# Kernel optimization log

Hardware: AMD Instinct MI355X
Metric: run time of the kernel (lower is better)

## Reference

```python
import jax, jax.numpy as jnp
import numpy as np

HIDDEN = 4096
NUM_HEADS = 32
HEAD_DIM = HIDDEN // NUM_HEADS  # 128
ROPE_THETA = 10000.0
B, S = 1, 2048


def setup_inputs() -> dict:
    key = jax.random.key(0)
    k1, k2, k3, k4, k5 = jax.random.split(key, 5)
    positions = jnp.broadcast_to(jnp.arange(S, dtype=jnp.int64), (B, S))
    hidden_states = jax.random.normal(k1, (B, S, HIDDEN), dtype=jnp.float32)
    scale = 1.0 / np.sqrt(HIDDEN)
    Wqkv = jax.random.normal(k2, (HIDDEN, 3 * HIDDEN), dtype=jnp.float32) * scale
    bqkv = jax.random.normal(k3, (3 * HIDDEN,), dtype=jnp.float32) * 0.01
    Wo = jax.random.normal(k4, (HIDDEN, HIDDEN), dtype=jnp.float32) * scale
    bo = jax.random.normal(k5, (HIDDEN,), dtype=jnp.float32) * 0.01
    return {"positions": positions, "hidden_states": hidden_states,
            "Wqkv": Wqkv, "bqkv": bqkv, "Wo": Wo, "bo": bo}


def _apply_rope(x, positions):
    # x: [B, S, H, D]; neox-style (rotate halves) rotary embedding
    half = HEAD_DIM // 2
    inv_freq = 1.0 / (ROPE_THETA ** (jnp.arange(0, HEAD_DIM, 2, dtype=jnp.float32) / HEAD_DIM))
    freqs = positions.astype(jnp.float32)[..., None] * inv_freq  # [B, S, half]
    cos = jnp.cos(freqs)[:, :, None, :]  # [B, S, 1, half]
    sin = jnp.sin(freqs)[:, :, None, :]
    x1, x2 = x[..., :half], x[..., half:]
    return jnp.concatenate([x1 * cos - x2 * sin, x2 * cos + x1 * sin], axis=-1)


def reference(positions, hidden_states, Wqkv, bqkv, Wo, bo):
    qkv = hidden_states @ Wqkv + bqkv  # [B, S, 3*HIDDEN]
    q, k, v = jnp.split(qkv, 3, axis=-1)
    q = q.reshape(B, S, NUM_HEADS, HEAD_DIM)
    k = k.reshape(B, S, NUM_HEADS, HEAD_DIM)
    v = v.reshape(B, S, NUM_HEADS, HEAD_DIM)
    q = _apply_rope(q, positions)
    k = _apply_rope(k, positions)
    scaling = HEAD_DIM ** -0.5
    scores = jnp.einsum('bshd,bthd->bhst', q, k) * scaling  # [B, H, S, S]
    causal = jnp.tril(jnp.ones((S, S), dtype=bool))
    scores = jnp.where(causal, scores, jnp.finfo(scores.dtype).min)
    attn = jax.nn.softmax(scores, axis=-1)
    out = jnp.einsum('bhst,bthd->bshd', attn, v).reshape(B, S, HIDDEN)
    return out @ Wo + bo
```

## Files before the change

kernel.cpp:

```cpp
#include <hip/hip_runtime.h>

using short8  = __attribute__((ext_vector_type(8))) short;
using floatx4 = __attribute__((ext_vector_type(4))) float;

__device__ inline float b2f(ushort u) {
  union { unsigned u; float f; } x; x.u = ((unsigned)u) << 16; return x.f;
}
__device__ inline ushort f2b(float f) {
  union { float f; unsigned u; } x; x.f = f;
  unsigned r = x.u + 0x7fffu + ((x.u >> 16) & 1u);
  return (ushort)(r >> 16);
}

__device__ __forceinline__ void gl_lds16(const void* g, void* l) {
  __builtin_amdgcn_global_load_lds(
      (const __attribute__((address_space(1))) unsigned*)(unsigned long long)g,
      (__attribute__((address_space(3))) unsigned*)(unsigned)(unsigned long long)l,
      16, 0, 0);
}

__global__ __launch_bounds__(256) void cvt_f32_bf16(
    const float* __restrict__ in, ushort* __restrict__ out, int n4) {
  const int i = blockIdx.x * 256 + threadIdx.x;
  if (i < n4) {
    const float4 v = ((const float4*)in)[i];
    ushort4 o;
    o.x = f2b(v.x); o.y = f2b(v.y); o.z = f2b(v.z); o.w = f2b(v.w);
    ((ushort4*)out)[i] = o;
  }
}

__global__ __launch_bounds__(256) void transpose_f32_bf16(
    const float* __restrict__ W, int ldw, ushort* __restrict__ Wt, int K) {
  __shared__ ushort tile[64 * 72];
  const int kb = blockIdx.y * 64, nb = blockIdx.x * 64;
  const int t = threadIdx.x;
  {
    const int tn = t & 63, tk4 = t >> 6;
#pragma unroll
    for (int i = 0; i < 16; ++i) {
      const int k = tk4 + i * 4;
      tile[k * 72 + tn] = f2b(W[(size_t)(kb + k) * ldw + (nb + tn)]);
    }
  }
  __syncthreads();
  {
    const int tk = t & 63, tn4 = t >> 6;
#pragma unroll
    for (int i = 0; i < 16; ++i) {
      const int n = tn4 + i * 4;
      Wt[(size_t)(nb + n) * K + (kb + tk)] = tile[tk * 72 + n];
    }
  }
}

__global__ __launch_bounds__(256) void transpose_v_bf16(
    const ushort* __restrict__ qkv, ushort* __restrict__ vT) {
  __shared__ ushort tile[64 * 68];
  const int s0 = blockIdx.y * 64, c0 = blockIdx.x * 64;
  const int t = threadIdx.x;
  {
    const int tc = t & 63, ts4 = t >> 6;
#pragma unroll
    for (int i = 0; i < 16; ++i) {
      const int s = ts4 + i * 4;
      tile[s * 68 + tc] = qkv[(size_t)(s0 + s) * 12288 + 8192 + c0 + tc];
    }
  }
  __syncthreads();
  {
    const int ts = t & 63, tc4 = t >> 6;
#pragma unroll
    for (int i = 0; i < 16; ++i) {
      const int c = tc4 + i * 4;
      vT[(size_t)(c0 + c) * 2048 + (s0 + ts)] = tile[ts * 68 + c];
    }
  }
}

template <bool F32OUT>
__global__ __launch_bounds__(256) void gemm_bt_bias(
    const ushort* __restrict__ A, const ushort* __restrict__ Bt,
    const float* __restrict__ bias, void* __restrict__ Cout,
    int ldc, int M, int N, int K) {
  __shared__ ushort sA[128 * 64];
  __shared__ ushort sB[128 * 64];
  const int tid = threadIdx.x;
  const int lane = tid & 63, w = tid >> 6;
  const int lm = lane & 15, lq = lane >> 4;
  const int wr = w >> 1, wc = w & 1;
  const int m0 = blockIdx.y * 128, n0 = blockIdx.x * 128;
  floatx4 acc[4][4] = {};

  const int srow = w * 32 + (lane >> 3);
  const int scol = (lane & 7) * 8;
  const ushort* Ag = A + (size_t)(m0 + srow) * K + scol;
  const ushort* Bg = Bt + (size_t)(n0 + srow) * K + scol;

  for (int k0 = 0; k0 < K; k0 += 64) {
    __syncthreads();
#pragma unroll
    for (int j = 0; j < 4; ++j) {
      gl_lds16(Ag + (size_t)j * 8 * K + k0, &sA[(w * 32 + j * 8) * 64]);
      gl_lds16(Bg + (size_t)j * 8 * K + k0, &sB[(w * 32 + j * 8) * 64]);
    }
    __syncthreads();
#pragma unroll
    for (int ks = 0; ks < 2; ++ks) {
      short8 af[4], bf[4];
#pragma unroll
      for (int i = 0; i < 4; ++i)
        af[i] = *(const short8*)&sA[(wr * 64 + i * 16 + lm) * 64 + ks * 32 + lq * 8];
#pragma unroll
      for (int j = 0; j < 4; ++j)
        bf[j] = *(const short8*)&sB[(wc * 64 + j * 16 + lm) * 64 + ks * 32 + lq * 8];
#pragma unroll
      for (int i = 0; i < 4; ++i)
#pragma unroll
        for (int j = 0; j < 4; ++j)
          acc[i][j] = __builtin_amdgcn_mfma_f32_16x16x32_bf16(af[i], bf[j], acc[i][j], 0, 0, 0);
    }
  }
#pragma unroll
  for (int i = 0; i < 4; ++i) {
#pragma unroll
    for (int j = 0; j < 4; ++j) {
      const int row = m0 + wr * 64 + i * 16 + lq * 4;
      const int col = n0 + wc * 64 + j * 16 + lm;
      const float bs = bias[col];
      if (F32OUT) {
        float* C = (float*)Cout;
#pragma unroll
        for (int r = 0; r < 4; ++r)
          C[(size_t)(row + r) * ldc + col] = acc[i][j][r] + bs;
      } else {
        ushort* C = (ushort*)Cout;
#pragma unroll
        for (int r = 0; r < 4; ++r)
          C[(size_t)(row + r) * ldc + col] = f2b(acc[i][j][r] + bs);
      }
    }
  }
}

__global__ __launch_bounds__(256) void rope_kernel(ushort* __restrict__ qkv) {
  const int s = blockIdx.x;
  const float pos = (float)s;
  for (int i = threadIdx.x; i < 2048; i += 256) {
    const int h = i >> 6, d = i & 63;
    const float inv_freq = exp2f(-(float)d * 0.20762050593045952f);
    const float f = pos * inv_freq;
    float sn, cs; sincosf(f, &sn, &cs);
    const size_t base = (size_t)s * 12288 + h * 128 + d;
    {
      float x1 = b2f(qkv[base]), x2 = b2f(qkv[base + 64]);
      qkv[base]      = f2b(x1 * cs - x2 * sn);
      qkv[base + 64] = f2b(x2 * cs + x1 * sn);
    }
    {
      const size_t kb = base + 4096;
      float x1 = b2f(qkv[kb]), x2 = b2f(qkv[kb + 64]);
      qkv[kb]      = f2b(x1 * cs - x2 * sn);
      qkv[kb + 64] = f2b(x2 * cs + x1 * sn);
    }
  }
}

__global__ __launch_bounds__(256) void flash_kernel(
    const ushort* __restrict__ qkv, const ushort* __restrict__ vT,
    ushort* __restrict__ attn) {
  constexpr int QKV = 12288;
  __shared__ ushort smem[20480];
  ushort* sK  = smem;
  ushort* sVt = smem + 8192;
  ushort* sP  = smem + 16384;

  const int h   = blockIdx.y;
  const int tid = threadIdx.x;
  const int lane = tid & 63, w = tid >> 6;
  const int lm = lane & 15, lq = lane >> 4;
  const int c16 = lane & 15, l4 = lane >> 4;
  const int c8  = lane & 7,  l3 = lane >> 3;
  const float sc = 0.08838834764831845f * 1.4426950408889634f;

  for (int qsel = 0; qsel < 2; ++qsel) {
    const int qt = qsel ? blockIdx.x : 31 - blockIdx.x;
    const int q0 = qt * 64;

    __syncthreads();
#pragma unroll
    for (int j = 0; j < 4; ++j) {
      const int row = w * 16 + j * 4 + l4;
      const int sw = c16 ^ (row & 7);
      gl_lds16(qkv + (size_t)(q0 + row) * QKV + h * 128 + sw * 8,
               &sK[(w * 16 + j * 4) * 128]);
    }
    __syncthreads();
    short8 aq[4];
#pragma unroll
    for (int kk = 0; kk < 4; ++kk)
      aq[kk] = *(const short8*)&sK[(w * 16 + lm) * 128 + (((kk * 4 + lq) ^ (lm & 7)) * 8)];

    floatx4 acco[8] = {};
    float mrun[4], lrun[4];
#pragma unroll
    for (int r = 0; r < 4; ++r) { mrun[r] = -1e30f; lrun[r] = 0.f; }

    const int nkv = qt + 1;
    for (int it = 0; it < nkv; ++it) {
      const int kv0 = it * 64;
      __syncthreads();
#pragma unroll
      for (int j = 0; j < 4; ++j) {
        const int row = w * 16 + j * 4 + l4;
        const int sw = c16 ^ (row & 7);
        gl_lds16(qkv + (size_t)(kv0 + row) * QKV + 4096 + h * 128 + sw * 8,
                 &sK[(w * 16 + j * 4) * 128]);
      }
#pragma unroll
      for (int j = 0; j < 4; ++j) {
        const int vrow = w * 32 + j * 8 + l3;
        const int sw = c8 ^ (vrow & 7);
        gl_lds16(vT + (size_t)(h * 128 + vrow) * 2048 + kv0 + sw * 8,
                 &sVt[(w * 32 + j * 8) * 64]);
      }
      __syncthreads();

      floatx4 accs[4] = {};
#pragma unroll
      for (int kk = 0; kk < 4; ++kk) {
        short8 bk[4];
#pragma unroll
        for (int nt = 0; nt < 4; ++nt)
          bk[nt] = *(const short8*)&sK[(nt * 16 + lm) * 128 + (((kk * 4 + lq) ^ (lm & 7)) * 8)];
#pragma unroll
        for (int nt = 0; nt < 4; ++nt)
          accs[nt] = __builtin_amdgcn_mfma_f32_16x16x32_bf16(aq[kk], bk[nt], accs[nt], 0, 0, 0);
      }

      const bool domask = (it == nkv - 1);
      float tmax[4];
#pragma unroll
      for (int r = 0; r < 4; ++r) tmax[r] = -1e30f;
#pragma unroll
      for (int nt = 0; nt < 4; ++nt)
#pragma unroll
        for (int r = 0; r < 4; ++r) {
          float v = accs[nt][r] * sc;
          if (domask) {
            const int qrow = q0 + w * 16 + lq * 4 + r;
            const int kcol = kv0 + nt * 16 + lm;
            if (kcol > qrow) v = -1e30f;
          }
          accs[nt][r] = v;
          tmax[r] = fmaxf(tmax[r], v);
        }
#pragma unroll
      for (int r = 0; r < 4; ++r) {
        float t = tmax[r];
#pragma unroll
        for (int off = 1; off < 16; off <<= 1) t = fmaxf(t, __shfl_xor(t, off, 64));
        const float mnew = fmaxf(mrun[r], t);
        const float alpha = exp2f(mrun[r] - mnew);
        mrun[r] = mnew;
        lrun[r] *= alpha;
#pragma unroll
        for (int nt = 0; nt < 8; ++nt) acco[nt][r] *= alpha;
      }
      float rsum[4] = {};
#pragma unroll
      for (int nt = 0; nt < 4; ++nt)
#pragma unroll
        for (int r = 0; r < 4; ++r) {
          const float p = exp2f(accs[nt][r] - mrun[r]);
          rsum[r] += p;
          sP[(w * 16 + lq * 4 + r) * 64 +
             (((2 * nt + (lm >> 3)) ^ ((lq * 4 + r) & 7)) * 8) + (lm & 7)] = f2b(p);
        }
#pragma unroll
      for (int r = 0; r < 4; ++r) {
        float t = rsum[r];
#pragma unroll
        for (int off = 1; off < 16; off <<= 1) t += __shfl_xor(t, off, 64);
        lrun[r] += t;
      }

#pragma unroll
      for (int ks = 0; ks < 2; ++ks) {
        const short8 ap = *(const short8*)&sP[(w * 16 + lm) * 64 + (((ks * 4 + lq) ^ (lm & 7)) * 8)];
#pragma unroll
        for (int nt = 0; nt < 8; ++nt) {
          const short8 bv = *(const short8*)&sVt[(nt * 16 + lm) * 64 + (((ks * 4 + lq) ^ (lm & 7)) * 8)];
          acco[nt] = __builtin_amdgcn_mfma_f32_16x16x32_bf16(ap, bv, acco[nt], 0, 0, 0);
        }
      }
    }

#pragma unroll
    for (int r = 0; r < 4; ++r) {
      const float inv = 1.0f / lrun[r];
      const int row = q0 + w * 16 + lq * 4 + r;
#pragma unroll
      for (int nt = 0; nt < 8; ++nt) {
        const int col = h * 128 + nt * 16 + lm;
        attn[(size_t)row * 4096 + col] = f2b(acco[nt][r] * inv);
      }
    }
  }
}

extern "C" void kernel_launch(void* const* d_in, const int* in_sizes, int n_in,
                              void* d_out, int out_size, void* d_ws, size_t ws_size,
                              hipStream_t stream) {
  const float* hidden = (const float*)d_in[1];
  const float* Wqkv   = (const float*)d_in[2];
  const float* bqkv   = (const float*)d_in[3];
  const float* Wo     = (const float*)d_in[4];
  const float* bo     = (const float*)d_in[5];

  ushort* ws   = (ushort*)d_ws;
  ushort* Wt   = ws;
  ushort* hb   = ws + (size_t)16777216;
  ushort* qkv  = ws + (size_t)25165824;
  ushort* attn = ws + (size_t)50331648;

  cvt_f32_bf16<<<8192, 256, 0, stream>>>(hidden, hb, 2097152);

  for (int c = 0; c < 3; ++c) {
    transpose_f32_bf16<<<dim3(64, 64), 256, 0, stream>>>(Wqkv + c * 4096, 12288, Wt, 4096);
    gemm_bt_bias<false><<<dim3(32, 16), 256, 0, stream>>>(
        hb, Wt, bqkv + c * 4096, (void*)(qkv + c * 4096), 12288, 2048, 4096, 4096);
  }

  rope_kernel<<<2048, 256, 0, stream>>>(qkv);
  transpose_v_bf16<<<dim3(64, 32), 256, 0, stream>>>(qkv, Wt);
  flash_kernel<<<dim3(16, 32), 256, 0, stream>>>(qkv, Wt, attn);

  transpose_f32_bf16<<<dim3(64, 64), 256, 0, stream>>>(Wo, 4096, Wt, 4096);
  gemm_bt_bias<true><<<dim3(32, 16), 256, 0, stream>>>(
      attn, Wt, bo, d_out, 4096, 2048, 4096, 4096);
}
```

Before: 870.1 us.

## Vectorize transposes and RoPE, give each flash block one query tile

The two transpose kernels switch to 16-byte vector global loads and stores, using an XOR-swizzled shared tile in place of padding. RoPE now handles 8 contiguous elements per thread with int4 loads and stores, with no strided loop. The flash kernel drops the pair of mirrored query tiles per block and launches twice as many blocks, one query tile each, ordered heaviest first. The last change raises parallelism but gives up the balanced per-block work of the pairing.

```diff
diff --git a/kernel.cpp b/kernel.cpp
--- a/kernel.cpp
+++ b/kernel.cpp
@@ -32,48 +32,69 @@
 
 __global__ __launch_bounds__(256) void transpose_f32_bf16(
     const float* __restrict__ W, int ldw, ushort* __restrict__ Wt, int K) {
-  __shared__ ushort tile[64 * 72];
+  __shared__ ushort tile[64 * 64];
   const int kb = blockIdx.y * 64, nb = blockIdx.x * 64;
   const int t = threadIdx.x;
   {
-    const int tn = t & 63, tk4 = t >> 6;
-#pragma unroll
-    for (int i = 0; i < 16; ++i) {
-      const int k = tk4 + i * 4;
-      tile[k * 72 + tn] = f2b(W[(size_t)(kb + k) * ldw + (nb + tn)]);
+    const int tn4 = t & 15;
+    const int tk  = t >> 4;
+#pragma unroll
+    for (int i = 0; i < 4; ++i) {
+      const int k = tk + i * 16;
+      const float4 v = *(const float4*)&W[(size_t)(kb + k) * ldw + nb + tn4 * 4];
+      ushort4 o; o.x = f2b(v.x); o.y = f2b(v.y); o.z = f2b(v.z); o.w = f2b(v.w);
+      const int c = tn4 ^ (k & 15);
+      *(ushort4*)&tile[k * 64 + c * 4] = o;
     }
   }
   __syncthreads();
   {
-    const int tk = t & 63, tn4 = t >> 6;
-#pragma unroll
-    for (int i = 0; i < 16; ++i) {
-      const int n = tn4 + i * 4;
-      Wt[(size_t)(nb + n) * K + (kb + tk)] = tile[tk * 72 + n];
+    const int kc = t & 7;
+    const int tn = t >> 3;
+#pragma unroll
+    for (int p = 0; p < 2; ++p) {
+      const int n = tn + p * 32;
+      union { int4 v; ushort u[8]; } o;
+#pragma unroll
+      for (int j = 0; j < 8; ++j) {
+        const int k = kc * 8 + j;
+        const int c = (n >> 2) ^ (k & 15);
+        o.u[j] = tile[k * 64 + c * 4 + (n & 3)];
+      }
+      *(int4*)&Wt[(size_t)(nb + n) * K + kb + kc * 8] = o.v;
     }
   }
 }
 
 __global__ __launch_bounds__(256) void transpose_v_bf16(
     const ushort* __restrict__ qkv, ushort* __restrict__ vT) {
-  __shared__ ushort tile[64 * 68];
+  __shared__ ushort tile[64 * 64];
   const int s0 = blockIdx.y * 64, c0 = blockIdx.x * 64;
   const int t = threadIdx.x;
   {
-    const int tc = t & 63, ts4 = t >> 6;
-#pragma unroll
-    for (int i = 0; i < 16; ++i) {
-      const int s = ts4 + i * 4;
-      tile[s * 68 + tc] = qkv[(size_t)(s0 + s) * 12288 + 8192 + c0 + tc];
+    const int tc8 = t & 7, ts = t >> 3;
+#pragma unroll
+    for (int p = 0; p < 2; ++p) {
+      const int s = ts + p * 32;
+      int4 x = *(const int4*)(qkv + (size_t)(s0 + s) * 12288 + 8192 + c0 + tc8 * 8);
+      const int c8 = tc8 ^ (s & 7) ^ ((s >> 3) & 7);
+      *(int4*)&tile[s * 64 + c8 * 8] = x;
     }
   }
   __syncthreads();
   {
-    const int ts = t & 63, tc4 = t >> 6;
-#pragma unroll
-    for (int i = 0; i < 16; ++i) {
-      const int c = tc4 + i * 4;
-      vT[(size_t)(c0 + c) * 2048 + (s0 + ts)] = tile[ts * 68 + c];
+    const int sc = t & 7, tc = t >> 3;
+#pragma unroll
+    for (int p = 0; p < 2; ++p) {
+      const int c = tc + p * 32;
+      union { int4 v; ushort u[8]; } o;
+#pragma unroll
+      for (int j = 0; j < 8; ++j) {
+        const int s = sc * 8 + j;
+        const int c8 = (c >> 3) ^ (s & 7) ^ ((s >> 3) & 7);
+        o.u[j] = tile[s * 64 + c8 * 8 + (c & 7)];
+      }
+      *(int4*)&vT[(size_t)(c0 + c) * 2048 + s0 + sc * 8] = o.v;
     }
   }
 }
@@ -146,24 +167,38 @@
 __global__ __launch_bounds__(256) void rope_kernel(ushort* __restrict__ qkv) {
   const int s = blockIdx.x;
   const float pos = (float)s;
-  for (int i = threadIdx.x; i < 2048; i += 256) {
-    const int h = i >> 6, d = i & 63;
-    const float inv_freq = exp2f(-(float)d * 0.20762050593045952f);
-    const float f = pos * inv_freq;
-    float sn, cs; sincosf(f, &sn, &cs);
-    const size_t base = (size_t)s * 12288 + h * 128 + d;
-    {
-      float x1 = b2f(qkv[base]), x2 = b2f(qkv[base + 64]);
-      qkv[base]      = f2b(x1 * cs - x2 * sn);
-      qkv[base + 64] = f2b(x2 * cs + x1 * sn);
-    }
-    {
-      const size_t kb = base + 4096;
-      float x1 = b2f(qkv[kb]), x2 = b2f(qkv[kb + 64]);
-      qkv[kb]      = f2b(x1 * cs - x2 * sn);
-      qkv[kb + 64] = f2b(x2 * cs + x1 * sn);
-    }
-  }
+  const int t = threadIdx.x;
+  const int h = t >> 3, d8 = (t & 7) * 8;
+  const size_t base = (size_t)s * 12288 + h * 128 + d8;
+  union U { int4 v; ushort u[8]; };
+  U q1, q2, k1, k2;
+  q1.v = *(const int4*)(qkv + base);
+  q2.v = *(const int4*)(qkv + base + 64);
+  k1.v = *(const int4*)(qkv + base + 4096);
+  k2.v = *(const int4*)(qkv + base + 4160);
+  float sn[8], cs[8];
+#pragma unroll
+  for (int j = 0; j < 8; ++j) {
+    const float inv_freq = exp2f(-(float)(d8 + j) * 0.20762050593045952f);
+    sincosf(pos * inv_freq, &sn[j], &cs[j]);
+  }
+  U o1, o2;
+#pragma unroll
+  for (int j = 0; j < 8; ++j) {
+    const float x1 = b2f(q1.u[j]), x2 = b2f(q2.u[j]);
+    o1.u[j] = f2b(x1 * cs[j] - x2 * sn[j]);
+    o2.u[j] = f2b(x2 * cs[j] + x1 * sn[j]);
+  }
+  *(int4*)(qkv + base)      = o1.v;
+  *(int4*)(qkv + base + 64) = o2.v;
+#pragma unroll
+  for (int j = 0; j < 8; ++j) {
+    const float x1 = b2f(k1.u[j]), x2 = b2f(k2.u[j]);
+    o1.u[j] = f2b(x1 * cs[j] - x2 * sn[j]);
+    o2.u[j] = f2b(x2 * cs[j] + x1 * sn[j]);
+  }
+  *(int4*)(qkv + base + 4096) = o1.v;
+  *(int4*)(qkv + base + 4160) = o2.v;
 }
 
 __global__ __launch_bounds__(256) void flash_kernel(
@@ -183,128 +218,125 @@
   const int c8  = lane & 7,  l3 = lane >> 3;
   const float sc = 0.08838834764831845f * 1.4426950408889634f;
 
-  for (int qsel = 0; qsel < 2; ++qsel) {
-    const int qt = qsel ? blockIdx.x : 31 - blockIdx.x;
-    const int q0 = qt * 64;
-
+  const int qt = 31 - blockIdx.x;
+  const int q0 = qt * 64;
+
+#pragma unroll
+  for (int j = 0; j < 4; ++j) {
+    const int row = w * 16 + j * 4 + l4;
+    const int sw = c16 ^ (row & 7);
+    gl_lds16(qkv + (size_t)(q0 + row) * QKV + h * 128 + sw * 8,
+             &sK[(w * 16 + j * 4) * 128]);
+  }
+  __syncthreads();
+  short8 aq[4];
+#pragma unroll
+  for (int kk = 0; kk < 4; ++kk)
+    aq[kk] = *(const short8*)&sK[(w * 16 + lm) * 128 + (((kk * 4 + lq) ^ (lm & 7)) * 8)];
+
+  floatx4 acco[8] = {};
+  float mrun[4], lrun[4];
+#pragma unroll
+  for (int r = 0; r < 4; ++r) { mrun[r] = -1e30f; lrun[r] = 0.f; }
+
+  const int nkv = qt + 1;
+  for (int it = 0; it < nkv; ++it) {
+    const int kv0 = it * 64;
     __syncthreads();
 #pragma unroll
     for (int j = 0; j < 4; ++j) {
       const int row = w * 16 + j * 4 + l4;
       const int sw = c16 ^ (row & 7);
-      gl_lds16(qkv + (size_t)(q0 + row) * QKV + h * 128 + sw * 8,
+      gl_lds16(qkv + (size_t)(kv0 + row) * QKV + 4096 + h * 128 + sw * 8,
                &sK[(w * 16 + j * 4) * 128]);
     }
+#pragma unroll
+    for (int j = 0; j < 4; ++j) {
+      const int vrow = w * 32 + j * 8 + l3;
+      const int sw = c8 ^ (vrow & 7);
+      gl_lds16(vT + (size_t)(h * 128 + vrow) * 2048 + kv0 + sw * 8,
+               &sVt[(w * 32 + j * 8) * 64]);
+    }
     __syncthreads();
-    short8 aq[4];
-#pragma unroll
-    for (int kk = 0; kk < 4; ++kk)
-      aq[kk] = *(const short8*)&sK[(w * 16 + lm) * 128 + (((kk * 4 + lq) ^ (lm & 7)) * 8)];
-
-    floatx4 acco[8] = {};
-    float mrun[4], lrun[4];
-#pragma unroll
-    for (int r = 0; r < 4; ++r) { mrun[r] = -1e30f; lrun[r] = 0.f; }
-
-    const int nkv = qt + 1;
-    for (int it = 0; it < nkv; ++it) {
-      const int kv0 = it * 64;
-      __syncthreads();
-#pragma unroll
-      for (int j = 0; j < 4; ++j) {
-        const int row = w * 16 + j * 4 + l4;
-        const int sw = c16 ^ (row & 7);
-        gl_lds16(qkv + (size_t)(kv0 + row) * QKV + 4096 + h * 128 + sw * 8,
-                 &sK[(w * 16 + j * 4) * 128]);
-      }
-#pragma unroll
-      for (int j = 0; j < 4; ++j) {
-        const int vrow = w * 32 + j * 8 + l3;
-        const int sw = c8 ^ (vrow & 7);
-        gl_lds16(vT + (size_t)(h * 128 + vrow) * 2048 + kv0 + sw * 8,
-                 &sVt[(w * 32 + j * 8) * 64]);
-      }
-      __syncthreads();
-
-      floatx4 accs[4] = {};
-#pragma unroll
-      for (int kk = 0; kk < 4; ++kk) {
-        short8 bk[4];
-#pragma unroll
-        for (int nt = 0; nt < 4; ++nt)
-          bk[nt] = *(const short8*)&sK[(nt * 16 + lm) * 128 + (((kk * 4 + lq) ^ (lm & 7)) * 8)];
-#pragma unroll
-        for (int nt = 0; nt < 4; ++nt)
-          accs[nt] = __builtin_amdgcn_mfma_f32_16x16x32_bf16(aq[kk], bk[nt], accs[nt], 0, 0, 0);
-      }
-
-      const bool domask = (it == nkv - 1);
-      float tmax[4];
-#pragma unroll
-      for (int r = 0; r < 4; ++r) tmax[r] = -1e30f;
+
+    floatx4 accs[4] = {};
+#pragma unroll
+    for (int kk = 0; kk < 4; ++kk) {
+      short8 bk[4];
 #pragma unroll
       for (int nt = 0; nt < 4; ++nt)
-#pragma unroll
-        for (int r = 0; r < 4; ++r) {
-          float v = accs[nt][r] * sc;
-          if (domask) {
-            const int qrow = q0 + w * 16 + lq * 4 + r;
-            const int kcol = kv0 + nt * 16 + lm;
-            if (kcol > qrow) v = -1e30f;
-          }
-          accs[nt][r] = v;
-          tmax[r] = fmaxf(tmax[r], v);
+        bk[nt] = *(const short8*)&sK[(nt * 16 + lm) * 128 + (((kk * 4 + lq) ^ (lm & 7)) * 8)];
+#pragma unroll
+      for (int nt = 0; nt < 4; ++nt)
+        accs[nt] = __builtin_amdgcn_mfma_f32_16x16x32_bf16(aq[kk], bk[nt], accs[nt], 0, 0, 0);
+    }
+
+    const bool domask = (it == nkv - 1);
+    float tmax[4];
+#pragma unroll
+    for (int r = 0; r < 4; ++r) tmax[r] = -1e30f;
+#pragma unroll
+    for (int nt = 0; nt < 4; ++nt)
+#pragma unroll
+      for (int r = 0; r < 4; ++r) {
+        float v = accs[nt][r] * sc;
+        if (domask) {
+          const int qrow = q0 + w * 16 + lq * 4 + r;
+          const int kcol = kv0 + nt * 16 + lm;
+          if (kcol > qrow) v = -1e30f;
         }
+        accs[nt][r] = v;
+        tmax[r] = fmaxf(tmax[r], v);
+      }
+#pragma unroll
+    for (int r = 0; r < 4; ++r) {
+      float t = tmax[r];
+#pragma unroll
+      for (int off = 1; off < 16; off <<= 1) t = fmaxf(t, __shfl_xor(t, off, 64));
+      const float mnew = fmaxf(mrun[r], t);
+      const float alpha = exp2f(mrun[r] - mnew);
+      mrun[r] = mnew;
+      lrun[r] *= alpha;
+#pragma unroll
+      for (int nt = 0; nt < 8; ++nt) acco[nt][r] *= alpha;
+    }
+    float rsum[4] = {};
+#pragma unroll
+    for (int nt = 0; nt < 4; ++nt)
 #pragma unroll
       for (int r = 0; r < 4; ++r) {
-        float t = tmax[r];
-#pragma unroll
-        for (int off = 1; off < 16; off <<= 1) t = fmaxf(t, __shfl_xor(t, off, 64));
-        const float mnew = fmaxf(mrun[r], t);
-        const float alpha = exp2f(mrun[r] - mnew);
-        mrun[r] = mnew;
-        lrun[r] *= alpha;
-#pragma unroll
-        for (int nt = 0; nt < 8; ++nt) acco[nt][r] *= alpha;
-      }
-      float rsum[4] = {};
-#pragma unroll
-      for (int nt = 0; nt < 4; ++nt)
-#pragma unroll
-        for (int r = 0; r < 4; ++r) {
-          const float p = exp2f(accs[nt][r] - mrun[r]);
-          rsum[r] += p;
-          sP[(w * 16 + lq * 4 + r) * 64 +
-             (((2 * nt + (lm >> 3)) ^ ((lq * 4 + r) & 7)) * 8) + (lm & 7)] = f2b(p);
-        }
-#pragma unroll
-      for (int r = 0; r < 4; ++r) {
-        float t = rsum[r];
-#pragma unroll
-        for (int off = 1; off < 16; off <<= 1) t += __shfl_xor(t, off, 64);
-        lrun[r] += t;
-      }
-
-#pragma unroll
-      for (int ks = 0; ks < 2; ++ks) {
-        const short8 ap = *(const short8*)&sP[(w * 16 + lm) * 64 + (((ks * 4 + lq) ^ (lm & 7)) * 8)];
-#pragma unroll
-        for (int nt = 0; nt < 8; ++nt) {
-          const short8 bv = *(const short8*)&sVt[(nt * 16 + lm) * 64 + (((ks * 4 + lq) ^ (lm & 7)) * 8)];
-          acco[nt] = __builtin_amdgcn_mfma_f32_16x16x32_bf16(ap, bv, acco[nt], 0, 0, 0);
-        }
-      }
-    }
-
+        const float p = exp2f(accs[nt][r] - mrun[r]);
+        rsum[r] += p;
+        sP[(w * 16 + lq * 4 + r) * 64 +
+           (((2 * nt + (lm >> 3)) ^ ((lq * 4 + r) & 7)) * 8) + (lm & 7)] = f2b(p);
+      }
 #pragma unroll
     for (int r = 0; r < 4; ++r) {
-      const float inv = 1.0f / lrun[r];
-      const int row = q0 + w * 16 + lq * 4 + r;
+      float t = rsum[r];
+#pragma unroll
+      for (int off = 1; off < 16; off <<= 1) t += __shfl_xor(t, off, 64);
+      lrun[r] += t;
+    }
+
+#pragma unroll
+    for (int ks = 0; ks < 2; ++ks) {
+      const short8 ap = *(const short8*)&sP[(w * 16 + lm) * 64 + (((ks * 4 + lq) ^ (lm & 7)) * 8)];
 #pragma unroll
       for (int nt = 0; nt < 8; ++nt) {
-        const int col = h * 128 + nt * 16 + lm;
-        attn[(size_t)row * 4096 + col] = f2b(acco[nt][r] * inv);
-      }
+        const short8 bv = *(const short8*)&sVt[(nt * 16 + lm) * 64 + (((ks * 4 + lq) ^ (lm & 7)) * 8)];
+        acco[nt] = __builtin_amdgcn_mfma_f32_16x16x32_bf16(ap, bv, acco[nt], 0, 0, 0);
+      }
+    }
+  }
+
+#pragma unroll
+  for (int r = 0; r < 4; ++r) {
+    const float inv = 1.0f / lrun[r];
+    const int row = q0 + w * 16 + lq * 4 + r;
+#pragma unroll
+    for (int nt = 0; nt < 8; ++nt) {
+      const int col = h * 128 + nt * 16 + lm;
+      attn[(size_t)row * 4096 + col] = f2b(acco[nt][r] * inv);
     }
   }
 }
@@ -334,7 +366,7 @@
 
   rope_kernel<<<2048, 256, 0, stream>>>(qkv);
   transpose_v_bf16<<<dim3(64, 32), 256, 0, stream>>>(qkv, Wt);
-  flash_kernel<<<dim3(16, 32), 256, 0, stream>>>(qkv, Wt, attn);
+  flash_kernel<<<dim3(32, 32), 256, 0, stream>>>(qkv, Wt, attn);
 
   transpose_f32_bf16<<<dim3(64, 64), 256, 0, stream>>>(Wo, 4096, Wt, 4096);
   gemm_bt_bias<true><<<dim3(32, 16), 256, 0, stream>>>(
```

New measurement: 942.1 us. +8.3%, slower.
